# Performance work log

Measured on AMD Instinct MI355X. Metric: run time of the kernel, lower is better.

The kernel has to match this reference:

```python
import jax, jax.numpy as jnp
import numpy as np

D_MODEL = 1024
NUM_HEADS = 16
D_K = D_MODEL // NUM_HEADS
B, S = 4, 2048


def setup_inputs() -> dict:
    key = jax.random.key(0)
    ks = jax.random.split(key, 12)
    scale = 1.0 / np.sqrt(D_MODEL)
    inp = {
        "q": jax.random.normal(ks[0], (B, S, D_MODEL), dtype=jnp.float32),
        "k": jax.random.normal(ks[1], (B, S, D_MODEL), dtype=jnp.float32),
        "v": jax.random.normal(ks[2], (B, S, D_MODEL), dtype=jnp.float32),
        "mask": jnp.ones((B, 1, 1, S), dtype=jnp.int32),
        "Wq": jax.random.normal(ks[3], (D_MODEL, D_MODEL), dtype=jnp.float32) * scale,
        "bq": jnp.zeros((D_MODEL,), dtype=jnp.float32),
        "Wk": jax.random.normal(ks[4], (D_MODEL, D_MODEL), dtype=jnp.float32) * scale,
        "bk": jnp.zeros((D_MODEL,), dtype=jnp.float32),
        "Wv": jax.random.normal(ks[5], (D_MODEL, D_MODEL), dtype=jnp.float32) * scale,
        "bv": jnp.zeros((D_MODEL,), dtype=jnp.float32),
        "Wo": jax.random.normal(ks[6], (D_MODEL, D_MODEL), dtype=jnp.float32) * scale,
        "bo": jnp.zeros((D_MODEL,), dtype=jnp.float32),
    }
    return inp


def reference(q, k, v, mask, Wq, bq, Wk, bk, Wv, bv, Wo, bo):
    b, s, d = q.shape
    # QKV projections (torch Linear: x @ W.T + b; here weights stored as (d,d) used as x @ W + b)
    query = (q @ Wq + bq).reshape(b, s, NUM_HEADS, D_K).transpose(0, 2, 1, 3)  # (b,h,s,dk)
    key_ = (k @ Wk + bk).reshape(b, s, NUM_HEADS, D_K).transpose(0, 2, 1, 3)
    value = (v @ Wv + bv).reshape(b, s, NUM_HEADS, D_K).transpose(0, 2, 1, 3)
    # full score matrix (b,h,s,s), scaled by sqrt(d_k)
    scores = jnp.einsum("bhqd,bhkd->bhqk", query, key_) / jnp.sqrt(jnp.float32(D_K))
    scores = jnp.where(mask == 0, jnp.float32(-jnp.inf), scores)
    attn = jax.nn.softmax(scores, axis=-1)
    # dropout p=0.0 (eval) -> identity
    out = jnp.einsum("bhqk,bhkd->bhqd", attn, value)  # (b,h,s,dk)
    out = out.transpose(0, 2, 1, 3).reshape(b, s, NUM_HEADS * D_K)
    return out @ Wo + bo
```

## Files before the change

### kernel.cpp

```cpp
#include <hip/hip_runtime.h>

typedef __attribute__((ext_vector_type(8)))  short  short8;
typedef __attribute__((ext_vector_type(4)))  short  short4v;
typedef __attribute__((ext_vector_type(4)))  float  f32x4;
typedef __attribute__((ext_vector_type(16))) float  f32x16;
typedef __attribute__((ext_vector_type(8)))  __bf16 bf8_t;
typedef __attribute__((ext_vector_type(4)))  __bf16 bf4_t;
typedef __attribute__((ext_vector_type(2)))  __bf16 bf2_t;
typedef __attribute__((ext_vector_type(4)))  unsigned uint4v;

#define DMODEL 1024
#define SEQ    2048
#define NB     4
#define NH     16
#define MTOT   (NB * SEQ)
#define SCALE_LOG2E 0.18033688011112042f
#define CSTRIDE 544
#define TSPAN   (8 * CSTRIDE)

static __device__ __forceinline__ ushort f2bf(float f) {
  union { float f; unsigned u; } v; v.f = f;
  unsigned r = v.u + 0x7fffu + ((v.u >> 16) & 1u);
  return (ushort)(r >> 16);
}

static __device__ __forceinline__ float fexp2(float x) {
#if __has_builtin(__builtin_amdgcn_exp2f)
  return __builtin_amdgcn_exp2f(x);
#else
  return __expf(x * 0.6931471805599453f);
#endif
}

static __device__ __forceinline__ f32x4 mfma32(short8 a, short8 b, f32x4 c) {
  return __builtin_amdgcn_mfma_f32_16x16x32_bf16(
      __builtin_bit_cast(bf8_t, a), __builtin_bit_cast(bf8_t, b), c, 0, 0, 0);
}

static __device__ __forceinline__ f32x16 mfma3232(short8 a, short8 b, f32x16 c) {
  return __builtin_amdgcn_mfma_f32_32x32x16_bf16(
      __builtin_bit_cast(bf8_t, a), __builtin_bit_cast(bf8_t, b), c, 0, 0, 0);
}

static __device__ __forceinline__ unsigned pk2(float a, float b) {
  bf2_t t; t[0] = (__bf16)a; t[1] = (__bf16)b;
  return __builtin_bit_cast(unsigned, t);
}

static __device__ __forceinline__ void plswap(unsigned& a, unsigned& b) {
  asm volatile("v_permlane32_swap_b32 %0, %1" : "+v"(a), "+v"(b));
}

static __device__ __forceinline__ void gl_lds16(const ushort* g, ushort* l) {
  __builtin_amdgcn_global_load_lds(
      (const __attribute__((address_space(1))) unsigned*)(unsigned long long)g,
      (__attribute__((address_space(3))) unsigned*)(unsigned long long)l,
      16, 0, 0);
}

__global__ __launch_bounds__(256) void cvt3_k(
    const float* __restrict__ q, const float* __restrict__ k,
    const float* __restrict__ v, ushort* __restrict__ qb,
    ushort* __restrict__ kb, ushort* __restrict__ vb) {
  const int z = blockIdx.y;
  const float* src = (z == 0) ? q : (z == 1) ? k : v;
  ushort* dst = (z == 0) ? qb : (z == 1) ? kb : vb;
  const size_t i = ((size_t)blockIdx.x * 256 + threadIdx.x) * 8;
  const float4 a0 = *(const float4*)&src[i];
  const float4 a1 = *(const float4*)&src[i + 4];
  bf8_t c;
  c[0] = (__bf16)a0.x; c[1] = (__bf16)a0.y; c[2] = (__bf16)a0.z; c[3] = (__bf16)a0.w;
  c[4] = (__bf16)a1.x; c[5] = (__bf16)a1.y; c[6] = (__bf16)a1.z; c[7] = (__bf16)a1.w;
  *(short8*)&dst[i] = __builtin_bit_cast(short8, c);
}

__global__ __launch_bounds__(64) void bias_k(const int* __restrict__ mask,
                                             float* __restrict__ biasf,
                                             unsigned* __restrict__ flags) {
  const int t = blockIdx.x * 64 + threadIdx.x;
  const int m = mask[t];
  biasf[t] = m ? 0.f : -1e30f;
  const unsigned long long bal = __ballot(m == 0);
  if (threadIdx.x == 0) flags[blockIdx.x] = (bal != 0ull) ? 1u : 0u;
}

__global__ __launch_bounds__(1024) void wtrans_k(
    const float* __restrict__ Wq, const float* __restrict__ Wk,
    const float* __restrict__ Wv, const float* __restrict__ Wo,
    ushort* __restrict__ Wt) {
  __shared__ float tile[32][33];
  const int z = blockIdx.z;
  const float* W = (z == 0) ? Wq : (z == 1) ? Wk : (z == 2) ? Wv : Wo;
  ushort* out = Wt + (size_t)z * DMODEL * DMODEL;
  const int tx = threadIdx.x, ty = threadIdx.y;
  const int n0 = blockIdx.x * 32, k0 = blockIdx.y * 32;
  tile[ty][tx] = W[(size_t)(k0 + ty) * DMODEL + n0 + tx];
  __syncthreads();
  out[(size_t)(n0 + ty) * DMODEL + k0 + tx] = f2bf(tile[tx][ty]);
}

template <int MODE>
__global__ __launch_bounds__(256) void gemm_k(
    const ushort* __restrict__ A, const ushort* __restrict__ Bt,
    const float* __restrict__ bias, void* __restrict__ out, const float scale) {
  __shared__ ushort Asm[128 * 32];
  __shared__ ushort Bsm[128 * 32];
  const int tid = threadIdx.x;
  const int wid = tid >> 6, lane = tid & 63;
  const int wr = wid >> 1, wc = wid & 1;
  const int lr = lane & 15, lg = lane >> 4;
  const int m0 = blockIdx.x * 128, n0 = blockIdx.y * 128;

  const int srow = lane >> 2, sslot = (lane & 3) * 8;
  const size_t gA0 = (size_t)(m0 + wid * 16 + srow) * DMODEL + sslot;
  const size_t gA1 = (size_t)(m0 + (wid + 4) * 16 + srow) * DMODEL + sslot;
  const size_t gB0 = (size_t)(n0 + wid * 16 + srow) * DMODEL + sslot;
  const size_t gB1 = (size_t)(n0 + (wid + 4) * 16 + srow) * DMODEL + sslot;
  ushort* lA0 = &Asm[wid * 512];
  ushort* lA1 = &Asm[(wid + 4) * 512];
  ushort* lB0 = &Bsm[wid * 512];
  ushort* lB1 = &Bsm[(wid + 4) * 512];

  f32x4 acc[4][4];
#pragma unroll
  for (int m = 0; m < 4; m++)
#pragma unroll
    for (int n = 0; n < 4; n++) acc[m][n] = (f32x4){0.f, 0.f, 0.f, 0.f};

  gl_lds16(&A[gA0], lA0);
  gl_lds16(&A[gA1], lA1);
  gl_lds16(&Bt[gB0], lB0);
  gl_lds16(&Bt[gB1], lB1);

  for (int ks = 0; ks < DMODEL / 32; ++ks) {
    __syncthreads();

    short8 af[4], bfr[4];
#pragma unroll
    for (int m = 0; m < 4; m++)
      af[m] = *(const short8*)&Asm[(wr * 64 + m * 16 + lr) * 32 + lg * 8];
#pragma unroll
    for (int n = 0; n < 4; n++)
      bfr[n] = *(const short8*)&Bsm[(wc * 64 + n * 16 + lr) * 32 + lg * 8];
#pragma unroll
    for (int m = 0; m < 4; m++)
#pragma unroll
      for (int n = 0; n < 4; n++) acc[m][n] = mfma32(af[m], bfr[n], acc[m][n]);

    __syncthreads();
    if (ks < DMODEL / 32 - 1) {
      const size_t ko = (size_t)(ks + 1) * 32;
      gl_lds16(&A[gA0 + ko], lA0);
      gl_lds16(&A[gA1 + ko], lA1);
      gl_lds16(&Bt[gB0 + ko], lB0);
      gl_lds16(&Bt[gB1 + ko], lB1);
    }
  }

  float bv4[4];
#pragma unroll
  for (int n = 0; n < 4; n++) bv4[n] = bias[n0 + wc * 64 + n * 16 + lr];
#pragma unroll
  for (int m = 0; m < 4; m++) {
    const int grb = m0 + wr * 64 + m * 16 + lg * 4;
#pragma unroll
    for (int n = 0; n < 4; n++) {
      const int gc = n0 + wc * 64 + n * 16 + lr;
      if (MODE == 2) {
        const int bb = grb >> 11, ss = grb & 2047, hh = gc >> 6, dk = gc & 63;
        bf4_t pk;
#pragma unroll
        for (int j = 0; j < 4; j++) pk[j] = (__bf16)((acc[m][n][j] + bv4[n]) * scale);
        const size_t addr = (((size_t)bb * NH + hh) * SEQ) * 64 +
                            (size_t)(ss >> 6) * 4096 + dk * 64 +
                            ((ss & 63) ^ ((dk & 7) * 8));
        *(short4v*)&((ushort*)out)[addr] = __builtin_bit_cast(short4v, pk);
      } else {
#pragma unroll
        for (int j = 0; j < 4; j++) {
          float val = (acc[m][n][j] + bv4[n]) * scale;
          int r = grb + j;
          if (MODE == 0) {
            int b = r >> 11, s = r & 2047, hh = gc >> 6, dk = gc & 63;
            ((ushort*)out)[((((size_t)b * NH + hh) * SEQ) + s) * 64 + dk] =
                __builtin_bit_cast(ushort, (__bf16)val);
          } else if (MODE == 3) {
            int b = r >> 11, s = r & 2047, hh = gc >> 6, dk = gc & 63;
            const size_t addr = (((size_t)b * NH + hh) * SEQ) * 64 +
                                (size_t)(s >> 6) * 4096 + (s & 63) * 64 +
                                (dk ^ ((s & 7) * 8));
            ((ushort*)out)[addr] = __builtin_bit_cast(ushort, (__bf16)val);
          } else {
            ((float*)out)[(size_t)r * DMODEL + gc] = val;
          }
        }
      }
    }
  }
}

__global__ __launch_bounds__(256) void attn_k(
    const ushort* __restrict__ Qp, const ushort* __restrict__ Kp,
    const ushort* __restrict__ Vt, const float* __restrict__ biasf,
    const unsigned* __restrict__ flags, ushort* __restrict__ ctx) {
  __shared__ ushort smem[4 * TSPAN];
  const int tid = threadIdx.x, w = tid >> 6, lane = tid & 63;
  const int q = lane & 31, hi = lane >> 5;
  const int n = blockIdx.x;
  const int xcd = n & 7, idx = n >> 3;
  const int bh = ((idx >> 4) << 3) | xcd;
  const int qt = idx & 15;
  const int b = bh >> 4, h = bh & 15;
  const int q0w = qt * 128 + w * 32;
  const ushort* Qh = Qp + (size_t)bh * SEQ * 64;
  const ushort* Kh = Kp + (size_t)bh * SEQ * 64;
  const ushort* Vh = Vt + (size_t)bh * SEQ * 64;
  const float* biasb = biasf + b * SEQ;
  const unsigned* flb = flags + b * 32;

  short8 qf[4];
#pragma unroll
  for (int c = 0; c < 4; c++)
    qf[c] = *(const short8*)&Qh[(size_t)(q0w + q) * 64 + c * 16 + hi * 8];

  const int xo = (q & 7) * 8;
  const int rbase = q * 64 + (q >> 3) * 32;
  int off[4];
#pragma unroll
  for (int c = 0; c < 4; c++) off[c] = rbase + ((c * 16 + hi * 8) ^ xo);

  const int sl = lane * 8;
  const int c0 = 2 * w, c1 = 2 * w + 1;

  f32x16 o0, o1;
#pragma unroll
  for (int r = 0; r < 16; r++) { o0[r] = 0.f; o1[r] = 0.f; }
  float l_run = 0.f;

  gl_lds16(&Kh[c0 * 512 + sl], &smem[c0 * CSTRIDE]);
  gl_lds16(&Kh[c1 * 512 + sl], &smem[c1 * CSTRIDE]);
  gl_lds16(&Vh[c0 * 512 + sl], &smem[2 * TSPAN + c0 * CSTRIDE]);
  gl_lds16(&Vh[c1 * 512 + sl], &smem[2 * TSPAN + c1 * CSTRIDE]);
  __syncthreads();

  for (int it = 0; it < 32; ++it) {
    const int cur = it & 1;
    if (it < 31) {
      const size_t tb = (size_t)(it + 1) * 4096;
      ushort* kd = &smem[(cur ^ 1) * TSPAN];
      ushort* vd = &smem[2 * TSPAN + (cur ^ 1) * TSPAN];
      gl_lds16(&Kh[tb + c0 * 512 + sl], &kd[c0 * CSTRIDE]);
      gl_lds16(&Kh[tb + c1 * 512 + sl], &kd[c1 * CSTRIDE]);
      gl_lds16(&Vh[tb + c0 * 512 + sl], &vd[c0 * CSTRIDE]);
      gl_lds16(&Vh[tb + c1 * 512 + sl], &vd[c1 * CSTRIDE]);
    }

    const ushort* kl = &smem[cur * TSPAN];
    const ushort* vl = &smem[2 * TSPAN + cur * TSPAN];

    f32x16 s0, s1;
#pragma unroll
    for (int r = 0; r < 16; r++) { s0[r] = 0.f; s1[r] = 0.f; }
#pragma unroll
    for (int c = 0; c < 4; c++)
      s0 = mfma3232(*(const short8*)&kl[off[c]], qf[c], s0);
#pragma unroll
    for (int c = 0; c < 4; c++)
      s1 = mfma3232(*(const short8*)&kl[off[c] + 2176], qf[c], s1);

    float p[32];
    if (flb[it]) {
      const float* bp = biasb + it * 64;
#pragma unroll
      for (int kt = 0; kt < 2; kt++)
#pragma unroll
        for (int g = 0; g < 4; g++) {
          const f32x4 ba = *(const f32x4*)&bp[kt * 32 + g * 8 + hi * 4];
#pragma unroll
          for (int j = 0; j < 4; j++)
            p[kt * 16 + g * 4 + j] =
                fexp2((kt ? s1[g * 4 + j] : s0[g * 4 + j]) + ba[j]);
        }
    } else {
#pragma unroll
      for (int r = 0; r < 16; r++) {
        p[r] = fexp2(s0[r]);
        p[16 + r] = fexp2(s1[r]);
      }
    }

    float a16[16], a8[8], a4[4];
#pragma unroll
    for (int i = 0; i < 16; i++) a16[i] = p[i] + p[16 + i];
#pragma unroll
    for (int i = 0; i < 8; i++) a8[i] = a16[i] + a16[8 + i];
#pragma unroll
    for (int i = 0; i < 4; i++) a4[i] = a8[i] + a8[4 + i];
    float ps = (a4[0] + a4[1]) + (a4[2] + a4[3]);
    ps += __shfl_xor(ps, 32);
    l_run += ps;

    short8 frag[4];
#pragma unroll
    for (int kb = 0; kb < 4; kb++) {
      unsigned X0 = pk2(p[8 * kb + 0], p[8 * kb + 1]);
      unsigned X1 = pk2(p[8 * kb + 2], p[8 * kb + 3]);
      unsigned Y0 = pk2(p[8 * kb + 4], p[8 * kb + 5]);
      unsigned Y1 = pk2(p[8 * kb + 6], p[8 * kb + 7]);
      plswap(X0, Y0);
      plswap(X1, Y1);
      frag[kb] = __builtin_bit_cast(short8, (uint4v){X0, X1, Y0, Y1});
    }

#pragma unroll
    for (int kb = 0; kb < 4; kb++) {
      o0 = mfma3232(*(const short8*)&vl[off[kb]], frag[kb], o0);
      o1 = mfma3232(*(const short8*)&vl[off[kb] + 2176], frag[kb], o1);
    }

    __syncthreads();
  }

  const float inv = 1.f / l_run;
  ushort* ow = &smem[w * 2176];
#pragma unroll
  for (int r = 0; r < 16; r++) {
    const int dk = (r & 3) + 8 * (r >> 2) + 4 * hi;
    ow[q * 68 + dk] = __builtin_bit_cast(ushort, (__bf16)(o0[r] * inv));
    ow[q * 68 + 32 + dk] = __builtin_bit_cast(ushort, (__bf16)(o1[r] * inv));
  }
  __syncthreads();
  const int sr = lane >> 4, dc = (lane & 15) * 4;
#pragma unroll
  for (int i = 0; i < 8; i++) {
    const int qq = i * 4 + sr;
    const short4v vv = *(const short4v*)&ow[qq * 68 + dc];
    *(short4v*)&ctx[((size_t)b * SEQ + q0w + qq) * DMODEL + h * 64 + dc] = vv;
  }
}

extern "C" void kernel_launch(void* const* d_in, const int* in_sizes, int n_in,
                              void* d_out, int out_size, void* d_ws,
                              size_t ws_size, hipStream_t stream) {
  const float* q    = (const float*)d_in[0];
  const float* k    = (const float*)d_in[1];
  const float* v    = (const float*)d_in[2];
  const int*   mask = (const int*)d_in[3];
  const float* Wq   = (const float*)d_in[4];
  const float* bq   = (const float*)d_in[5];
  const float* Wk   = (const float*)d_in[6];
  const float* bk   = (const float*)d_in[7];
  const float* Wv   = (const float*)d_in[8];
  const float* bv   = (const float*)d_in[9];
  const float* Wo   = (const float*)d_in[10];
  const float* bo   = (const float*)d_in[11];

  char* p = (char*)d_ws;
  ushort* Wt = (ushort*)p; p += (size_t)4 * DMODEL * DMODEL * 2;
  ushort* Qp = (ushort*)p; p += (size_t)MTOT * DMODEL * 2;
  ushort* Kp = (ushort*)p; p += (size_t)MTOT * DMODEL * 2;
  ushort* Vb = (ushort*)p; p += (size_t)MTOT * DMODEL * 2;
  ushort* qb = (ushort*)p; p += (size_t)MTOT * DMODEL * 2;
  ushort* kb = (ushort*)p; p += (size_t)MTOT * DMODEL * 2;
  ushort* vb = (ushort*)p; p += (size_t)MTOT * DMODEL * 2;
  float*  biasf = (float*)p; p += (size_t)NB * SEQ * 4;
  unsigned* flags = (unsigned*)p;
  ushort* ctx = qb;

  wtrans_k<<<dim3(32, 32, 4), dim3(32, 32), 0, stream>>>(Wq, Wk, Wv, Wo, Wt);
  bias_k<<<NB * SEQ / 64, 64, 0, stream>>>(mask, biasf, flags);
  cvt3_k<<<dim3(MTOT * DMODEL / (256 * 8), 3), 256, 0, stream>>>(q, k, v, qb,
                                                                 kb, vb);

  dim3 gg(MTOT / 128, DMODEL / 128);
  gemm_k<0><<<gg, 256, 0, stream>>>(qb, Wt, bq, Qp, SCALE_LOG2E);
  gemm_k<3><<<gg, 256, 0, stream>>>(kb, Wt + (size_t)DMODEL * DMODEL, bk, Kp, 1.f);
  gemm_k<2><<<gg, 256, 0, stream>>>(vb, Wt + (size_t)2 * DMODEL * DMODEL, bv, Vb, 1.f);

  attn_k<<<1024, 256, 0, stream>>>(Qp, Kp, Vb, biasf, flags, ctx);

  gemm_k<1><<<gg, 256, 0, stream>>>(ctx, Wt + (size_t)3 * DMODEL * DMODEL, bo,
                                    d_out, 1.f);
}
```

Baseline: 231.2 us.

## Batch QKV projections into one launch, retune attention LDS stride, add MFMA priority

The three QKV projection GEMMs are merged into a single launch with a z grid dimension, so 1536 blocks run concurrently instead of three serialized launches of 512. The attention kernel's LDS tile stride changes from 544 to 528, with row offsets recomputed to match, which alters bank-conflict behaviour and shrinks shared memory use. s_setprio is raised around the MFMA sections so matrix work is favoured across waves. The output GEMM becomes its own non-templated kernel, and runtime z branches in the epilogue add a little per-thread overhead.

```diff
diff --git a/kernel.cpp b/kernel.cpp
--- a/kernel.cpp
+++ b/kernel.cpp
@@ -15,7 +15,7 @@
 #define NH     16
 #define MTOT   (NB * SEQ)
 #define SCALE_LOG2E 0.18033688011112042f
-#define CSTRIDE 544
+#define CSTRIDE 528
 #define TSPAN   (8 * CSTRIDE)
 
 static __device__ __forceinline__ ushort f2bf(float f) {
@@ -99,64 +99,63 @@
   out[(size_t)(n0 + ty) * DMODEL + k0 + tx] = f2bf(tile[tx][ty]);
 }
 
-template <int MODE>
-__global__ __launch_bounds__(256) void gemm_k(
-    const ushort* __restrict__ A, const ushort* __restrict__ Bt,
-    const float* __restrict__ bias, void* __restrict__ out, const float scale) {
-  __shared__ ushort Asm[128 * 32];
-  __shared__ ushort Bsm[128 * 32];
-  const int tid = threadIdx.x;
-  const int wid = tid >> 6, lane = tid & 63;
-  const int wr = wid >> 1, wc = wid & 1;
-  const int lr = lane & 15, lg = lane >> 4;
-  const int m0 = blockIdx.x * 128, n0 = blockIdx.y * 128;
-
-  const int srow = lane >> 2, sslot = (lane & 3) * 8;
-  const size_t gA0 = (size_t)(m0 + wid * 16 + srow) * DMODEL + sslot;
-  const size_t gA1 = (size_t)(m0 + (wid + 4) * 16 + srow) * DMODEL + sslot;
-  const size_t gB0 = (size_t)(n0 + wid * 16 + srow) * DMODEL + sslot;
-  const size_t gB1 = (size_t)(n0 + (wid + 4) * 16 + srow) * DMODEL + sslot;
-  ushort* lA0 = &Asm[wid * 512];
-  ushort* lA1 = &Asm[(wid + 4) * 512];
-  ushort* lB0 = &Bsm[wid * 512];
-  ushort* lB1 = &Bsm[(wid + 4) * 512];
-
-  f32x4 acc[4][4];
-#pragma unroll
-  for (int m = 0; m < 4; m++)
-#pragma unroll
-    for (int n = 0; n < 4; n++) acc[m][n] = (f32x4){0.f, 0.f, 0.f, 0.f};
-
-  gl_lds16(&A[gA0], lA0);
-  gl_lds16(&A[gA1], lA1);
-  gl_lds16(&Bt[gB0], lB0);
-  gl_lds16(&Bt[gB1], lB1);
-
-  for (int ks = 0; ks < DMODEL / 32; ++ks) {
-    __syncthreads();
-
-    short8 af[4], bfr[4];
-#pragma unroll
-    for (int m = 0; m < 4; m++)
-      af[m] = *(const short8*)&Asm[(wr * 64 + m * 16 + lr) * 32 + lg * 8];
-#pragma unroll
-    for (int n = 0; n < 4; n++)
-      bfr[n] = *(const short8*)&Bsm[(wc * 64 + n * 16 + lr) * 32 + lg * 8];
-#pragma unroll
-    for (int m = 0; m < 4; m++)
-#pragma unroll
-      for (int n = 0; n < 4; n++) acc[m][n] = mfma32(af[m], bfr[n], acc[m][n]);
-
-    __syncthreads();
-    if (ks < DMODEL / 32 - 1) {
-      const size_t ko = (size_t)(ks + 1) * 32;
-      gl_lds16(&A[gA0 + ko], lA0);
-      gl_lds16(&A[gA1 + ko], lA1);
-      gl_lds16(&Bt[gB0 + ko], lB0);
-      gl_lds16(&Bt[gB1 + ko], lB1);
-    }
-  }
-
+#define GEMM_BODY(A, Bt)                                                        \
+  __shared__ ushort Asm[128 * 32];                                              \
+  __shared__ ushort Bsm[128 * 32];                                              \
+  const int tid = threadIdx.x;                                                  \
+  const int wid = tid >> 6, lane = tid & 63;                                    \
+  const int wr = wid >> 1, wc = wid & 1;                                        \
+  const int lr = lane & 15, lg = lane >> 4;                                     \
+  const int m0 = blockIdx.x * 128, n0 = blockIdx.y * 128;                       \
+  const int srow = lane >> 2, sslot = (lane & 3) * 8;                           \
+  const size_t gA0 = (size_t)(m0 + wid * 16 + srow) * DMODEL + sslot;           \
+  const size_t gA1 = (size_t)(m0 + (wid + 4) * 16 + srow) * DMODEL + sslot;     \
+  const size_t gB0 = (size_t)(n0 + wid * 16 + srow) * DMODEL + sslot;           \
+  const size_t gB1 = (size_t)(n0 + (wid + 4) * 16 + srow) * DMODEL + sslot;     \
+  ushort* lA0 = &Asm[wid * 512];                                                \
+  ushort* lA1 = &Asm[(wid + 4) * 512];                                          \
+  ushort* lB0 = &Bsm[wid * 512];                                                \
+  ushort* lB1 = &Bsm[(wid + 4) * 512];                                          \
+  f32x4 acc[4][4];                                                              \
+  _Pragma("unroll") for (int m = 0; m < 4; m++)                                 \
+      _Pragma("unroll") for (int n = 0; n < 4; n++)                             \
+          acc[m][n] = (f32x4){0.f, 0.f, 0.f, 0.f};                              \
+  gl_lds16(&A[gA0], lA0);                                                       \
+  gl_lds16(&A[gA1], lA1);                                                       \
+  gl_lds16(&Bt[gB0], lB0);                                                      \
+  gl_lds16(&Bt[gB1], lB1);                                                      \
+  for (int ks = 0; ks < DMODEL / 32; ++ks) {                                    \
+    __syncthreads();                                                            \
+    short8 af[4], bfr[4];                                                       \
+    _Pragma("unroll") for (int m = 0; m < 4; m++) af[m] =                       \
+        *(const short8*)&Asm[(wr * 64 + m * 16 + lr) * 32 + lg * 8];            \
+    _Pragma("unroll") for (int n = 0; n < 4; n++) bfr[n] =                      \
+        *(const short8*)&Bsm[(wc * 64 + n * 16 + lr) * 32 + lg * 8];            \
+    _Pragma("unroll") for (int m = 0; m < 4; m++)                               \
+        _Pragma("unroll") for (int n = 0; n < 4; n++)                           \
+            acc[m][n] = mfma32(af[m], bfr[n], acc[m][n]);                       \
+    __syncthreads();                                                            \
+    if (ks < DMODEL / 32 - 1) {                                                 \
+      const size_t ko = (size_t)(ks + 1) * 32;                                  \
+      gl_lds16(&A[gA0 + ko], lA0);                                              \
+      gl_lds16(&A[gA1 + ko], lA1);                                              \
+      gl_lds16(&Bt[gB0 + ko], lB0);                                             \
+      gl_lds16(&Bt[gB1 + ko], lB1);                                             \
+    }                                                                           \
+  }
+
+__global__ __launch_bounds__(256) void gemmqkv_k(
+    const ushort* __restrict__ qb, const ushort* __restrict__ kb,
+    const ushort* __restrict__ vb, const ushort* __restrict__ Wt,
+    const float* __restrict__ bq, const float* __restrict__ bk,
+    const float* __restrict__ bv, ushort* __restrict__ Qp,
+    ushort* __restrict__ Kp, ushort* __restrict__ Vb) {
+  const int z = blockIdx.z;
+  const ushort* A = (z == 0) ? qb : (z == 1) ? kb : vb;
+  const ushort* Bt = Wt + (size_t)z * DMODEL * DMODEL;
+  const float* bias = (z == 0) ? bq : (z == 1) ? bk : bv;
+  GEMM_BODY(A, Bt)
+  const float scale = (z == 0) ? SCALE_LOG2E : 1.f;
   float bv4[4];
 #pragma unroll
   for (int n = 0; n < 4; n++) bv4[n] = bias[n0 + wc * 64 + n * 16 + lr];
@@ -166,35 +165,53 @@
 #pragma unroll
     for (int n = 0; n < 4; n++) {
       const int gc = n0 + wc * 64 + n * 16 + lr;
-      if (MODE == 2) {
-        const int bb = grb >> 11, ss = grb & 2047, hh = gc >> 6, dk = gc & 63;
+      const int hh = gc >> 6, dk = gc & 63;
+      if (z == 2) {
+        const int bb = grb >> 11, ss = grb & 2047;
         bf4_t pk;
 #pragma unroll
-        for (int j = 0; j < 4; j++) pk[j] = (__bf16)((acc[m][n][j] + bv4[n]) * scale);
+        for (int j = 0; j < 4; j++) pk[j] = (__bf16)(acc[m][n][j] + bv4[n]);
         const size_t addr = (((size_t)bb * NH + hh) * SEQ) * 64 +
                             (size_t)(ss >> 6) * 4096 + dk * 64 +
                             ((ss & 63) ^ ((dk & 7) * 8));
-        *(short4v*)&((ushort*)out)[addr] = __builtin_bit_cast(short4v, pk);
+        *(short4v*)&Vb[addr] = __builtin_bit_cast(short4v, pk);
       } else {
 #pragma unroll
         for (int j = 0; j < 4; j++) {
-          float val = (acc[m][n][j] + bv4[n]) * scale;
-          int r = grb + j;
-          if (MODE == 0) {
-            int b = r >> 11, s = r & 2047, hh = gc >> 6, dk = gc & 63;
-            ((ushort*)out)[((((size_t)b * NH + hh) * SEQ) + s) * 64 + dk] =
+          const float val = (acc[m][n][j] + bv4[n]) * scale;
+          const int r = grb + j;
+          const int b = r >> 11, s = r & 2047;
+          if (z == 0) {
+            Qp[((((size_t)b * NH + hh) * SEQ) + s) * 64 + dk] =
                 __builtin_bit_cast(ushort, (__bf16)val);
-          } else if (MODE == 3) {
-            int b = r >> 11, s = r & 2047, hh = gc >> 6, dk = gc & 63;
+          } else {
             const size_t addr = (((size_t)b * NH + hh) * SEQ) * 64 +
                                 (size_t)(s >> 6) * 4096 + (s & 63) * 64 +
                                 (dk ^ ((s & 7) * 8));
-            ((ushort*)out)[addr] = __builtin_bit_cast(ushort, (__bf16)val);
-          } else {
-            ((float*)out)[(size_t)r * DMODEL + gc] = val;
+            Kp[addr] = __builtin_bit_cast(ushort, (__bf16)val);
           }
         }
       }
+    }
+  }
+}
+
+__global__ __launch_bounds__(256) void gemmo_k(
+    const ushort* __restrict__ Ain, const ushort* __restrict__ Btin,
+    const float* __restrict__ bias, float* __restrict__ out) {
+  GEMM_BODY(Ain, Btin)
+  float bv4[4];
+#pragma unroll
+  for (int n = 0; n < 4; n++) bv4[n] = bias[n0 + wc * 64 + n * 16 + lr];
+#pragma unroll
+  for (int m = 0; m < 4; m++) {
+    const int grb = m0 + wr * 64 + m * 16 + lg * 4;
+#pragma unroll
+    for (int n = 0; n < 4; n++) {
+      const int gc = n0 + wc * 64 + n * 16 + lr;
+#pragma unroll
+      for (int j = 0; j < 4; j++)
+        out[(size_t)(grb + j) * DMODEL + gc] = acc[m][n][j] + bv4[n];
     }
   }
 }
@@ -224,7 +241,7 @@
     qf[c] = *(const short8*)&Qh[(size_t)(q0w + q) * 64 + c * 16 + hi * 8];
 
   const int xo = (q & 7) * 8;
-  const int rbase = q * 64 + (q >> 3) * 32;
+  const int rbase = (q >> 3) * CSTRIDE + (q & 7) * 64;
   int off[4];
 #pragma unroll
   for (int c = 0; c < 4; c++) off[c] = rbase + ((c * 16 + hi * 8) ^ xo);
@@ -261,12 +278,14 @@
     f32x16 s0, s1;
 #pragma unroll
     for (int r = 0; r < 16; r++) { s0[r] = 0.f; s1[r] = 0.f; }
+    __builtin_amdgcn_s_setprio(1);
 #pragma unroll
     for (int c = 0; c < 4; c++)
       s0 = mfma3232(*(const short8*)&kl[off[c]], qf[c], s0);
 #pragma unroll
     for (int c = 0; c < 4; c++)
-      s1 = mfma3232(*(const short8*)&kl[off[c] + 2176], qf[c], s1);
+      s1 = mfma3232(*(const short8*)&kl[off[c] + 4 * CSTRIDE], qf[c], s1);
+    __builtin_amdgcn_s_setprio(0);
 
     float p[32];
     if (flb[it]) {
@@ -312,11 +331,13 @@
       frag[kb] = __builtin_bit_cast(short8, (uint4v){X0, X1, Y0, Y1});
     }
 
+    __builtin_amdgcn_s_setprio(1);
 #pragma unroll
     for (int kb = 0; kb < 4; kb++) {
       o0 = mfma3232(*(const short8*)&vl[off[kb]], frag[kb], o0);
-      o1 = mfma3232(*(const short8*)&vl[off[kb] + 2176], frag[kb], o1);
-    }
+      o1 = mfma3232(*(const short8*)&vl[off[kb] + 4 * CSTRIDE], frag[kb], o1);
+    }
+    __builtin_amdgcn_s_setprio(0);
 
     __syncthreads();
   }
@@ -372,13 +393,11 @@
   cvt3_k<<<dim3(MTOT * DMODEL / (256 * 8), 3), 256, 0, stream>>>(q, k, v, qb,
                                                                  kb, vb);
 
-  dim3 gg(MTOT / 128, DMODEL / 128);
-  gemm_k<0><<<gg, 256, 0, stream>>>(qb, Wt, bq, Qp, SCALE_LOG2E);
-  gemm_k<3><<<gg, 256, 0, stream>>>(kb, Wt + (size_t)DMODEL * DMODEL, bk, Kp, 1.f);
-  gemm_k<2><<<gg, 256, 0, stream>>>(vb, Wt + (size_t)2 * DMODEL * DMODEL, bv, Vb, 1.f);
+  gemmqkv_k<<<dim3(MTOT / 128, DMODEL / 128, 3), 256, 0, stream>>>(
+      qb, kb, vb, Wt, bq, bk, bv, Qp, Kp, Vb);
 
   attn_k<<<1024, 256, 0, stream>>>(Qp, Kp, Vb, biasf, flags, ctx);
 
-  gemm_k<1><<<gg, 256, 0, stream>>>(ctx, Wt + (size_t)3 * DMODEL * DMODEL, bo,
-                                    d_out, 1.f);
-}
+  gemmo_k<<<dim3(MTOT / 128, DMODEL / 128), 256, 0, stream>>>(
+      ctx, Wt + (size_t)3 * DMODEL * DMODEL, bo, (float*)d_out);
+}
```

Result: slower. 238.2 us (+3.1%).
